# Optimization experiments

Hardware: AMD Instinct MI355X
Metric: run time of the kernel (lower is better)

Reference implementation:

```python
import jax, jax.numpy as jnp
import numpy as np

B, S, C = 16, 1024, 8
V, D, E, H, R = 50257, 512, 8, 512, 32
F, RT, CD, Q = 1024, 512, 64, 128
EPS = 1e-6


def _normalize(x):
    n = jnp.maximum(jnp.linalg.norm(x, axis=-1, keepdims=True), EPS)
    return x / n


def _fake_quantize(x):
    # F.normalize then straight-through int8 quant on the unit vector
    xn = _normalize(x)
    q = jnp.clip(jnp.round(xn * 127.0), -127.0, 127.0)
    return xn + jax.lax.stop_gradient(q / 127.0 - xn)


def setup_inputs() -> dict:
    key = jax.random.key(0)
    ks = iter(jax.random.split(key, 64))

    def w(shape, s=0.02):
        return (jax.random.normal(next(ks), shape, dtype=jnp.float32) * s)

    inp = {}
    inp['prefix_tokens'] = jax.random.randint(next(ks), (B, S), 0, V, dtype=jnp.int32)
    inp['chunk_inputs'] = jax.random.randint(next(ks), (B, C), 0, V, dtype=jnp.int32)
    inp['chunk_targets'] = jax.random.randint(next(ks), (B, C), 0, V, dtype=jnp.int32)
    inp['next_chunk_tokens'] = jax.random.randint(next(ks), (B, C), 0, V, dtype=jnp.int32)

    inp['emb'] = w((V, D))
    # stacked per-expert AffineExpert params
    inp['Wa'] = w((E, D, H)); inp['ba'] = jnp.zeros((E, H), jnp.float32)
    inp['Wg'] = w((E, D, R)); inp['bg'] = jnp.zeros((E, R), jnp.float32)
    inp['Wu'] = w((E, D, H)); inp['bu'] = jnp.zeros((E, H), jnp.float32)
    inp['u_mat'] = w((E, H, R)); inp['v_mat'] = w((E, H, R))
    inp['Wp'] = w((E, H, F)); inp['bp'] = jnp.zeros((E, F), jnp.float32)
    # gate MLP
    inp['Wg1'] = w((D, D)); inp['bg1'] = jnp.zeros((D,), jnp.float32)
    inp['Wg2'] = w((D, E)); inp['bg2'] = jnp.zeros((E,), jnp.float32)
    # query / target / key / code-expansion / write-code
    inp['Wq'] = w((F, Q)); inp['bq'] = jnp.zeros((Q,), jnp.float32)
    inp['Wt1'] = w((2 * D, RT)); inp['bt1'] = jnp.zeros((RT,), jnp.float32)
    inp['Wt2'] = w((RT, RT)); inp['bt2'] = jnp.zeros((RT,), jnp.float32)
    inp['Wk'] = w((RT, Q)); inp['bk'] = jnp.zeros((Q,), jnp.float32)
    inp['Web'] = w((CD, RT))  # expansion_basis (no bias)
    inp['Wwc'] = w((F, CD)); inp['bwc'] = jnp.zeros((CD,), jnp.float32)
    # ctx MLP
    inp['Wc1'] = w((2 * F, F)); inp['bc1'] = jnp.zeros((F,), jnp.float32)
    inp['Wc2'] = w((F, F)); inp['bc2'] = jnp.zeros((F,), jnp.float32)
    # chunk decoder
    inp['chunk_pos'] = w((C, F))
    inp['Wci'] = w((D + F, F)); inp['bci'] = jnp.zeros((F,), jnp.float32)
    inp['Wm1'] = w((F, F)); inp['bm1'] = jnp.zeros((F,), jnp.float32)
    inp['Wm2'] = w((F, F)); inp['bm2'] = jnp.zeros((F,), jnp.float32)
    inp['Wlm'] = w((F, V)); inp['blm'] = jnp.zeros((V,), jnp.float32)
    return inp


def _expert_scan(x, Wa, ba, Wg, bg, Wu, bu, u_mat, v_mat):
    # x: [B,S,D]; precompute all per-step projections as one big GEMM each,
    # leading axis = time for lax.scan. A,U: [S,E,B,H], G: [S,E,B,R]
    A = jax.nn.sigmoid(jnp.einsum('bsd,edh->sebh', x, Wa) + ba[None, :, None, :])
    G = jnp.einsum('bsd,edr->sebr', x, Wg) + bg[None, :, None, :]
    U = jnp.einsum('bsd,edh->sebh', x, Wu) + bu[None, :, None, :]

    def step(state, inp):  # state: [E,B,H]
        a, g, u = inp
        low = jnp.einsum('ebh,ehr->ebr', state, v_mat) * g
        state = a * state + u + jnp.einsum('ebr,ehr->ebh', low, u_mat)
        return state, None

    state0 = jnp.zeros((E, B, H), x.dtype)
    state, _ = jax.lax.scan(step, state0, (A, G, U))
    return state  # [E,B,H]


def reference(prefix_tokens, chunk_inputs, chunk_targets, next_chunk_tokens,
              emb, Wa, ba, Wg, bg, Wu, bu, u_mat, v_mat, Wp, bp,
              Wg1, bg1, Wg2, bg2, Wq, bq, Wt1, bt1, Wt2, bt2, Wk, bk,
              Web, Wwc, bwc, Wc1, bc1, Wc2, bc2,
              chunk_pos, Wci, bci, Wm1, bm1, Wm2, bm2, Wlm, blm):
    # ---- encode_prefix ----
    prefix_emb = emb[prefix_tokens]                       # [B,S,D]
    summary = prefix_emb.mean(axis=1)                     # [B,D]
    gate_probs = jax.nn.softmax(jax.nn.silu(summary @ Wg1 + bg1) @ Wg2 + bg2, axis=-1)  # [B,E]
    states = _expert_scan(prefix_emb, Wa, ba, Wg, bg, Wu, bu, u_mat, v_mat)             # [E,B,H]
    proj = jnp.einsum('ebh,ehf->ebf', states, Wp) + bp[:, None, :]                       # [E,B,F]
    fused = jnp.einsum('ebf,be->bf', proj, gate_probs)    # [B,F]

    # ---- query / target / key ----
    q_st = _fake_quantize(fused @ Wq + bq)                # [B,Q]
    chunk_emb = emb[chunk_targets].mean(axis=1)           # [B,D]
    next_emb = emb[next_chunk_tokens].mean(axis=1)        # [B,D]
    t_in = jnp.concatenate([chunk_emb, next_emb], axis=-1)
    target_state = _normalize(jax.nn.silu(t_in @ Wt1 + bt1) @ Wt2 + bt2)  # [B,RT]
    target_k_st = _fake_quantize(target_state @ Wk + bk)  # [B,Q]

    # ---- read_context (bank=None path -> zero read) ----
    zero_read = jnp.zeros_like(fused)
    c_in = jnp.concatenate([fused, zero_read], axis=-1)
    ctx = jax.nn.silu(c_in @ Wc1 + bc1) @ Wc2 + bc2       # [B,F]

    # ---- write_from_ctx ----
    write_codes = ctx @ Wwc + bwc                         # [B,CD]
    write_state = _normalize(write_codes @ Web)           # [B,RT]
    write_k_st = _fake_quantize(write_state @ Wk + bk)    # [B,Q]

    # ---- decode_chunk ----
    tok = emb[chunk_inputs]                               # [B,C,D]
    ctx_rep = jnp.broadcast_to(ctx[:, None, :], (B, C, F))
    hidden = jnp.concatenate([tok, ctx_rep], axis=-1) @ Wci + bci + chunk_pos[None]  # [B,C,F]
    hidden = jax.nn.silu(hidden @ Wm1 + bm1) @ Wm2 + bm2
    logits = hidden @ Wlm + blm                           # [B,C,V]

    # ---- losses ----
    logp = jax.nn.log_softmax(logits, axis=-1)
    token_loss = -jnp.take_along_axis(logp, chunk_targets[..., None], axis=-1)[..., 0]
    loss_nll = token_loss.mean()
    sim = (q_st @ target_k_st.T) / jnp.sqrt(jnp.float32(Q))  # [B,B]
    return logits, loss_nll, sim, write_k_st
```

## Files before the change

kernel.cpp:

```cpp
#include <hip/hip_runtime.h>
#include <math.h>

constexpr int BB = 16;
constexpr int SS = 1024;
constexpr int CC = 8;
constexpr int VV = 50257;
constexpr int DD = 512;
constexpr int EE = 8;
constexpr int HH = 512;
constexpr int RR = 32;
constexpr int FF = 1024;
constexpr int RTd = 512;
constexpr int CDd = 64;
constexpr int QQ = 128;
constexpr int SCH = 128;

typedef short bf16x8 __attribute__((ext_vector_type(8)));
typedef float f32x4 __attribute__((ext_vector_type(4)));

__device__ __forceinline__ float sigm(float x){ return 1.0f/(1.0f+expf(-x)); }

__device__ __forceinline__ unsigned short f2bf(float f){
  unsigned int u = __float_as_uint(f);
  u += 0x7fff + ((u>>16)&1);
  return (unsigned short)(u>>16);
}
__device__ __forceinline__ float bf2f(unsigned short h){
  return __uint_as_float(((unsigned int)h)<<16);
}

__device__ __forceinline__ void gload16(unsigned short* l, const unsigned short* g){
  __builtin_amdgcn_global_load_lds(
      (const __attribute__((address_space(1))) unsigned int*)(g),
      (__attribute__((address_space(3))) unsigned int*)(l), 16, 0, 0);
}

__global__ __launch_bounds__(256) void gather_pack(const int* __restrict__ toks,
    const float* __restrict__ emb, unsigned short* __restrict__ xp){
  int id = blockIdx.x*256 + threadIdx.x;
  int b = id >> 17;
  int rem = id & 131071;
  int c = rem >> 14;
  int rem2 = rem & 16383;
  int kc = rem2 >> 10;
  int pb = rem2 & 1023;
  int row = pb >> 3, q = pb & 7;
  int v = q ^ (row & 7);
  int kq = v >> 1, h = v & 1;
  int tok = toks[b*SS + c*128 + row];
  const float* src = emb + (size_t)tok*DD + kc*32 + kq*8;
  unsigned short o[8];
  #pragma unroll
  for (int j=0;j<8;j++){
    float f = src[j];
    unsigned short hi = f2bf(f);
    o[j] = h ? f2bf(f - bf2f(hi)) : hi;
  }
  ushort4* dst = (ushort4*)(xp + (size_t)id*8);
  dst[0] = make_ushort4(o[0],o[1],o[2],o[3]);
  dst[1] = make_ushort4(o[4],o[5],o[6],o[7]);
}

__global__ __launch_bounds__(512) void colsum_part(const int* __restrict__ toks,
    const float* __restrict__ emb, float* __restrict__ part){
  int b = blockIdx.y, j = blockIdx.x, d = threadIdx.x;
  float s = 0.f;
  for (int k=0;k<64;k++){
    int tok = toks[b*SS + j*64 + k];
    s += emb[(size_t)tok*DD + d];
  }
  part[(b*16 + j)*DD + d] = s;
}
__global__ __launch_bounds__(512) void colsum_final(const float* __restrict__ part,
                                                    float* __restrict__ summary){
  int b = blockIdx.x, d = threadIdx.x;
  float s = 0.f;
  for (int j=0;j<16;j++) s += part[(b*16 + j)*DD + d];
  summary[b*DD + d] = s * (1.0f/1024.0f);
}

__global__ __launch_bounds__(128) void gate_h1(const float* __restrict__ summary,
                                               const float* __restrict__ Wg1,
                                               const float* __restrict__ bg1,
                                               float* __restrict__ h1){
  int t = threadIdx.x; int j = blockIdx.x*128 + t;
  __shared__ float sm[16*512];
  for (int idx=t; idx<8192; idx+=128) sm[idx] = summary[idx];
  __syncthreads();
  float acc[16] = {0};
  for (int d=0; d<DD; d++){
    float w = Wg1[d*DD + j];
    #pragma unroll
    for (int b2=0;b2<16;b2++) acc[b2] += sm[b2*DD + d]*w;
  }
  #pragma unroll
  for (int b2=0;b2<16;b2++){ float v = acc[b2] + bg1[j]; h1[b2*DD + j] = v*sigm(v); }
}
__global__ __launch_bounds__(128) void gate_probs_k(const float* __restrict__ h1,
                                                    const float* __restrict__ Wg2,
                                                    const float* __restrict__ bg2,
                                                    float* __restrict__ gate){
  int t = threadIdx.x;
  int b = t>>3, e = t&7;
  float acc = bg2[e];
  for (int d=0; d<DD; d++) acc += h1[b*DD + d]*Wg2[d*EE + e];
  __shared__ float lg[16][8];
  lg[b][e] = acc;
  __syncthreads();
  if (e==0){
    float m = -3.4e38f;
    for (int i=0;i<8;i++) m = fmaxf(m, lg[b][i]);
    float s = 0.f; float ex[8];
    for (int i=0;i<8;i++){ ex[i] = expf(lg[b][i]-m); s += ex[i]; }
    for (int i=0;i<8;i++) gate[b*EE + i] = ex[i]/s;
  }
}

__global__ __launch_bounds__(256) void convT_pack_au(const float* __restrict__ Wa,
    const float* __restrict__ Wu, unsigned short* __restrict__ WPackAU){
  const int ec = blockIdx.x;
  const int kc = blockIdx.y;
  const int e = ec >> 3, ct = ec & 7;
  __shared__ float ta[32][64];
  __shared__ float tu[32][64];
  const int t = threadIdx.x;
  for (int i=0;i<8;i++){
    int id = t + i*256;
    int c = id & 63, kk = id >> 6;
    size_t src = ((size_t)e*DD + kc*32 + kk)*HH + ct*64 + c;
    ta[kk][c] = Wa[src];
    tu[kk][c] = Wu[src];
  }
  __syncthreads();
  unsigned short* o = WPackAU + ((size_t)ec*16 + kc)*8192;
  for (int i=0;i<8;i++){
    int idx4 = t + i*256;
    int blk = idx4 >> 1, half = idx4 & 1;
    int a = blk >> 8, kq = (blk >> 6) & 3, c = blk & 63;
    const float* src = (a >> 1) ? &tu[0][0] : &ta[0][0];
    unsigned short s4[4];
    #pragma unroll
    for (int j2=0;j2<4;j2++){
      int j = half*4 + j2;
      float f = src[(kq*8 + j)*64 + c];
      unsigned short hi = f2bf(f);
      s4[j2] = (a & 1) ? f2bf(f - bf2f(hi)) : hi;
    }
    *(ushort4*)&o[(size_t)idx4*4] = make_ushort4(s4[0],s4[1],s4[2],s4[3]);
  }
}
__global__ __launch_bounds__(256) void convT_pack_g(const float* __restrict__ Wge,
    unsigned short* __restrict__ WPackG){
  const int gt = blockIdx.x;
  const int kc = blockIdx.y;
  __shared__ float tg[32][64];
  const int t = threadIdx.x;
  for (int i=0;i<8;i++){
    int id = t + i*256;
    int c = id & 63, kk = id >> 6;
    int gcol = gt*64 + c;
    tg[kk][c] = Wge[((size_t)(gcol>>5)*DD + kc*32 + kk)*RR + (gcol & 31)];
  }
  __syncthreads();
  unsigned short* o = WPackG + ((size_t)gt*16 + kc)*4096;
  for (int i=0;i<4;i++){
    int idx4 = t + i*256;
    int blk = idx4 >> 1, half = idx4 & 1;
    int a = blk >> 8, kq = (blk >> 6) & 3, c = blk & 63;
    unsigned short s4[4];
    #pragma unroll
    for (int j2=0;j2<4;j2++){
      int j = half*4 + j2;
      float f = tg[kq*8 + j][c];
      unsigned short hi = f2bf(f);
      s4[j2] = a ? f2bf(f - bf2f(hi)) : hi;
    }
    *(ushort4*)&o[(size_t)idx4*4] = make_ushort4(s4[0],s4[1],s4[2],s4[3]);
  }
}

__global__ __launch_bounds__(512, 2) void aug_scan(
    const unsigned short* __restrict__ xp,
    const unsigned short* __restrict__ WPackAU, const unsigned short* __restrict__ WPackG,
    const float* __restrict__ ba, const float* __restrict__ bu, const float* __restrict__ bge,
    float* __restrict__ Aw, float* __restrict__ Uw, float* __restrict__ Gw,
    const float* __restrict__ Ar, const float* __restrict__ Ur, const float* __restrict__ Gr,
    const float* __restrict__ v_mat, const float* __restrict__ u_mat,
    float* __restrict__ states,
    int s0, int do_aug, int do_scan)
{
  __shared__ __align__(16) unsigned short lds[32768];
  const int t = threadIdx.x;
  const int xcd  = blockIdx.x & 7;
  const int slot = blockIdx.x >> 3;

  if (slot < 16){
    if (!do_scan) return;
    const int e = xcd;
    const int b = slot;
    const int r = t & 31, grp = t >> 5;
    float* stf   = (float*)lds;
    float* partf = (float*)lds + 1024;
    float* lowf  = (float*)lds + 1312;
    float vreg[32];
    #pragma unroll
    for (int i=0;i<32;i++) vreg[i] = v_mat[((size_t)e*HH + grp*32 + i)*RR + r];
    float ureg[32];
    {
      const float4* up = (const float4*)(u_mat + ((size_t)e*HH + t)*RR);
      #pragma unroll
      for (int j=0;j<8;j++){
        float4 v4 = up[j];
        ureg[j*4+0]=v4.x; ureg[j*4+1]=v4.y; ureg[j*4+2]=v4.z; ureg[j*4+3]=v4.w;
      }
    }
    const size_t sbase = ((size_t)e*BB + b)*HH + t;
    const size_t abase = ((size_t)e*BB + b)*SCH*HH + t;
    const size_t gbase = ((size_t)e*BB + b)*SCH*RR + r;
    float streg = states[sbase];
    stf[t] = streg;
    float a0 = Ar[abase], u0 = Ur[abase];
    float g0 = (t < 32) ? Gr[gbase] : 0.f;
    float a1 = Ar[abase + HH], u1 = Ur[abase + HH];
    float g1 = (t < 32) ? Gr[gbase + RR] : 0.f;
    __syncthreads();
    int cur = 0;
    for (int s=0; s<SCH; s++){
      float a2 = 0.f, u2 = 0.f, g2 = 0.f;
      if (s+2 < SCH){
        a2 = Ar[abase + (size_t)(s+2)*HH];
        u2 = Ur[abase + (size_t)(s+2)*HH];
        if (t < 32) g2 = Gr[gbase + (size_t)(s+2)*RR];
      }
      {
        const float* sp = &stf[cur*512 + grp*32];
        float p0=0.f,p1=0.f,p2=0.f,p3=0.f;
        #pragma unroll
        for (int i=0;i<8;i++){
          p0 += sp[i]     *vreg[i];
          p1 += sp[8+i]   *vreg[8+i];
          p2 += sp[16+i]  *vreg[16+i];
          p3 += sp[24+i]  *vreg[24+i];
        }
        float p = (p0+p1)+(p2+p3);
        p += __shfl_xor(p, 32, 64);
        if ((t & 32) == 0) partf[r*9 + (grp>>1)] = p;
      }
      __syncthreads();
      if (t < 32){
        float ss2 = 0.f;
        #pragma unroll
        for (int j=0;j<8;j++) ss2 += partf[t*9 + j];
        lowf[t] = ss2 * g0;
      }
      __syncthreads();
      {
        float q0=0.f,q1=0.f,q2=0.f,q3=0.f;
        #pragma unroll
        for (int i=0;i<8;i++){
          q0 += lowf[i]   *ureg[i];
          q1 += lowf[8+i] *ureg[8+i];
          q2 += lowf[16+i]*ureg[16+i];
          q3 += lowf[24+i]*ureg[24+i];
        }
        streg = a0*streg + u0 + ((q0+q1)+(q2+q3));
      }
      stf[(cur^1)*512 + t] = streg;
      cur ^= 1;
      a0=a1; u0=u1; g0=g1; a1=a2; u1=u2; g1=g2;
      __syncthreads();
    }
    states[sbase] = streg;
    return;
  }

  if (!do_aug) return;
  const int s2 = slot - 16;
  int b, ct;
  if (s2 < 128){ ct = xcd*8 + (s2 & 7); b = s2 >> 3; }
  else         { ct = 64 + (xcd >> 1);  b = ((xcd & 1) << 3) + (s2 - 128); }
  const int lane = t & 63, wv = t >> 6;
  const int cix = s0 >> 7;
  const unsigned short* xpc = xp + (((size_t)(b*8 + cix)) << 17);
  const int wo = wv*64;

  f32x4 acc[2][4] = {};
  const int cl15 = lane & 15;

  if (ct < 64){
    const int e = ct >> 3;
    const int c0 = (ct & 7)*64;
    const unsigned short* wpc = WPackAU + (((size_t)ct) << 17);
    const int strip = wv & 3;
    const int mode  = wv >> 2;
    const int kq4 = lane >> 4;
    const int rr0 = strip*32 + cl15, rr1 = rr0 + 16;
    const int qh = (kq4*2) ^ (rr0 & 7);
    const int ql = (kq4*2+1) ^ (rr0 & 7);
    const int ab = mode*512;

#define STAGE_AU(BUF, KC) { \
    unsigned short* XB_ = lds + (BUF)*16384; \
    unsigned short* WB_ = XB_ + 8192; \
    const unsigned short* gx = xpc + (KC)*8192; \
    const unsigned short* gw = wpc + (KC)*8192; \
    gload16(XB_ + wo*8,        gx + (size_t)(wo + lane)*8); \
    gload16(XB_ + (512+wo)*8,  gx + (size_t)(512 + wo + lane)*8); \
    gload16(WB_ + wo*8,        gw + (size_t)(wo + lane)*8); \
    gload16(WB_ + (512+wo)*8,  gw + (size_t)(512 + wo + lane)*8); }

    STAGE_AU(0, 0)
    asm volatile("s_waitcnt vmcnt(0)" ::: "memory");
    __builtin_amdgcn_s_barrier();
    __builtin_amdgcn_sched_barrier(0);
    int cur = 0;
    for (int kc=0; kc<16; kc++){
      if (kc < 15) STAGE_AU(cur^1, kc+1)
      const unsigned short* XB = lds + cur*16384;
      const unsigned short* WB = XB + 8192;
      bf16x8 ah0 = *(const bf16x8*)&XB[(rr0*8 + qh)*8];
      bf16x8 al0 = *(const bf16x8*)&XB[(rr0*8 + ql)*8];
      bf16x8 ah1 = *(const bf16x8*)&XB[(rr1*8 + qh)*8];
      bf16x8 al1 = *(const bf16x8*)&XB[(rr1*8 + ql)*8];
      #pragma unroll
      for (int cf=0; cf<4; cf++){
        const int cc = cf*16 + cl15;
        bf16x8 bh = *(const bf16x8*)&WB[(ab + kq4*64 + cc)*8];
        bf16x8 bl = *(const bf16x8*)&WB[(ab + 256 + kq4*64 + cc)*8];
        acc[0][cf] = __builtin_amdgcn_mfma_f32_16x16x32_bf16(ah0, bh, acc[0][cf], 0,0,0);
        acc[0][cf] = __builtin_amdgcn_mfma_f32_16x16x32_bf16(ah0, bl, acc[0][cf], 0,0,0);
        acc[0][cf] = __builtin_amdgcn_mfma_f32_16x16x32_bf16(al0, bh, acc[0][cf], 0,0,0);
        acc[1][cf] = __builtin_amdgcn_mfma_f32_16x16x32_bf16(ah1, bh, acc[1][cf], 0,0,0);
        acc[1][cf] = __builtin_amdgcn_mfma_f32_16x16x32_bf16(ah1, bl, acc[1][cf], 0,0,0);
        acc[1][cf] = __builtin_amdgcn_mfma_f32_16x16x32_bf16(al1, bh, acc[1][cf], 0,0,0);
      }
      __builtin_amdgcn_sched_barrier(0);
      asm volatile("s_waitcnt vmcnt(0)" ::: "memory");
      __builtin_amdgcn_s_barrier();
      __builtin_amdgcn_sched_barrier(0);
      cur ^= 1;
    }
#undef STAGE_AU
    const int r4 = (lane >> 4) * 4;
    const size_t obase = ((size_t)e*BB + b)*SCH*HH;
    #pragma unroll
    for (int rf=0; rf<2; rf++){
      #pragma unroll
      for (int cf=0; cf<4; cf++){
        #pragma unroll
        for (int i=0;i<4;i++){
          int sl = strip*32 + rf*16 + r4 + i;
          int ce = c0 + cf*16 + cl15;
          float v = acc[rf][cf][i];
          if (mode == 0){
            v += ba[e*HH + ce];
            v = sigm(v);
            Aw[obase + (size_t)sl*HH + ce] = v;
          } else {
            v += bu[e*HH + ce];
            Uw[obase + (size_t)sl*HH + ce] = v;
          }
        }
      }
    }
  } else {
    const int gt = ct - 64;
    const int c0 = gt*64;
    const unsigned short* wpc = WPackG + (((size_t)gt) << 16);
    const int kq4 = lane >> 4;
    const int rr0 = wv*16 + cl15;
    const int qh = (kq4*2) ^ (rr0 & 7);
    const int ql = (kq4*2+1) ^ (rr0 & 7);

#define STAGE_G(BUF, KC) { \
    unsigned short* XB_ = lds + (BUF)*16384; \
    unsigned short* WB_ = XB_ + 8192; \
    const unsigned short* gx = xpc + (KC)*8192; \
    const unsigned short* gw = wpc + (KC)*4096; \
    gload16(XB_ + wo*8,        gx + (size_t)(wo + lane)*8); \
    gload16(XB_ + (512+wo)*8,  gx + (size_t)(512 + wo + lane)*8); \
    gload16(WB_ + wo*8,        gw + (size_t)(wo + lane)*8); }

    STAGE_G(0, 0)
    asm volatile("s_waitcnt vmcnt(0)" ::: "memory");
    __builtin_amdgcn_s_barrier();
    __builtin_amdgcn_sched_barrier(0);
    int cur = 0;
    for (int kc=0; kc<16; kc++){
      if (kc < 15) STAGE_G(cur^1, kc+1)
      const unsigned short* XB = lds + cur*16384;
      const unsigned short* WB = XB + 8192;
      bf16x8 ah0 = *(const bf16x8*)&XB[(rr0*8 + qh)*8];
      bf16x8 al0 = *(const bf16x8*)&XB[(rr0*8 + ql)*8];
      #pragma unroll
      for (int cf=0; cf<4; cf++){
        const int cc = cf*16 + cl15;
        bf16x8 bh = *(const bf16x8*)&WB[(kq4*64 + cc)*8];
        bf16x8 bl = *(const bf16x8*)&WB[(256 + kq4*64 + cc)*8];
        acc[0][cf] = __builtin_amdgcn_mfma_f32_16x16x32_bf16(ah0, bh, acc[0][cf], 0,0,0);
        acc[0][cf] = __builtin_amdgcn_mfma_f32_16x16x32_bf16(ah0, bl, acc[0][cf], 0,0,0);
        acc[0][cf] = __builtin_amdgcn_mfma_f32_16x16x32_bf16(al0, bh, acc[0][cf], 0,0,0);
      }
      __builtin_amdgcn_sched_barrier(0);
      asm volatile("s_waitcnt vmcnt(0)" ::: "memory");
      __builtin_amdgcn_s_barrier();
      __builtin_amdgcn_sched_barrier(0);
      cur ^= 1;
    }
#undef STAGE_G
    const int r4 = (lane >> 4) * 4;
    #pragma unroll
    for (int cf=0; cf<4; cf++){
      #pragma unroll
      for (int i=0;i<4;i++){
        int sl = wv*16 + r4 + i;
        int g = c0 + cf*16 + cl15;
        int ee = g >> 5, r2 = g & 31;
        float v = acc[0][cf][i] + bge[ee*RR + r2];
        Gw[((size_t)ee*BB + b)*SCH*RR + (size_t)sl*RR + r2] = v;
      }
    }
  }
}

__global__ __launch_bounds__(128) void proj_partial(const float* __restrict__ states,
    const float* __restrict__ Wp, const float* __restrict__ gate, float* __restrict__ pf){
  int fc = blockIdx.x, e = blockIdx.y, t = threadIdx.x;
  __shared__ float stl[16*512];
  for (int idx=t; idx<8192; idx+=128) stl[idx] = states[(size_t)e*8192 + idx];
  __syncthreads();
  int f = fc*128 + t;
  float acc[16] = {0};
  for (int h=0; h<HH; h++){
    float w = Wp[((size_t)e*HH + h)*FF + f];
    #pragma unroll
    for (int b2=0;b2<16;b2++) acc[b2] += stl[b2*HH + h]*w;
  }
  #pragma unroll
  for (int b2=0;b2<16;b2++) pf[((size_t)(e*16 + b2))*FF + f] = gate[b2*EE + e]*acc[b2];
}
__global__ __launch_bounds__(256) void fuse_reduce(const float* __restrict__ pf,
    const float* __restrict__ gate, const float* __restrict__ bp, float* __restrict__ fused){
  int idx = blockIdx.x*256 + threadIdx.x;
  int b = idx >> 10, f = idx & 1023;
  float s = 0.f;
  #pragma unroll
  for (int e=0;e<8;e++) s += pf[((size_t)(e*16 + b))*FF + f] + gate[b*EE + e]*bp[e*FF + f];
  fused[idx] = s;
}

__global__ __launch_bounds__(128) void fq_linear(const float* __restrict__ in, int Kin,
    const float* __restrict__ W, const float* __restrict__ bias, float* __restrict__ out){
  int b = blockIdx.x, t = threadIdx.x;
  __shared__ float xin[1024];
  __shared__ float red[2];
  for (int k=t;k<Kin;k+=128) xin[k] = in[(size_t)b*Kin + k];
  __syncthreads();
  float acc = bias[t];
  for (int k=0;k<Kin;k++) acc += xin[k]*W[k*QQ + t];
  float ss = acc*acc;
  #pragma unroll
  for (int off=32; off; off>>=1) ss += __shfl_xor(ss, off, 64);
  if ((t&63)==0) red[t>>6] = ss;
  __syncthreads();
  float n = fmaxf(sqrtf(red[0]+red[1]), 1e-6f);
  float xn = acc / n;
  float q = fminf(fmaxf(rintf(xn*127.0f), -127.0f), 127.0f) * (1.0f/127.0f);
  out[b*QQ + t] = q;
}

__global__ __launch_bounds__(512) void chunk_means(const int* __restrict__ ct,
    const int* __restrict__ nct, const float* __restrict__ emb, float* __restrict__ tin){
  int b = blockIdx.x, d = threadIdx.x;
  float ce=0.f, ne=0.f;
  for (int c=0;c<CC;c++){
    ce += emb[(size_t)ct[b*CC+c]*DD + d];
    ne += emb[(size_t)nct[b*CC+c]*DD + d];
  }
  tin[b*1024 + d] = ce*0.125f;
  tin[b*1024 + 512 + d] = ne*0.125f;
}

__global__ __launch_bounds__(512) void target_state_kernel(const float* __restrict__ tin,
    const float* __restrict__ Wt1, const float* __restrict__ bt1,
    const float* __restrict__ Wt2, const float* __restrict__ bt2, float* __restrict__ outts){
  int b = blockIdx.x, t = threadIdx.x;
  __shared__ float xin[1024];
  __shared__ float h1[512];
  __shared__ float red[8];
  for (int k=t;k<1024;k+=512) xin[k] = tin[b*1024 + k];
  __syncthreads();
  float acc = bt1[t];
  for (int k=0;k<1024;k++) acc += xin[k]*Wt1[k*RTd + t];
  acc = acc*sigm(acc);
  h1[t] = acc;
  __syncthreads();
  float y = bt2[t];
  for (int k=0;k<512;k++) y += h1[k]*Wt2[k*RTd + t];
  float ss = y*y;
  #pragma unroll
  for (int off=32; off; off>>=1) ss += __shfl_xor(ss, off, 64);
  if ((t&63)==0) red[t>>6] = ss;
  __syncthreads();
  float tot = 0.f;
  #pragma unroll
  for (int i=0;i<8;i++) tot += red[i];
  float n = fmaxf(sqrtf(tot), 1e-6f);
  outts[b*RTd + t] = y/n;
}

__global__ __launch_bounds__(512) void write_state_kernel(const float* __restrict__ ctx,
    const float* __restrict__ Wwc, const float* __restrict__ bwc,
    const float* __restrict__ Web, float* __restrict__ wsn){
  int b = blockIdx.x, t = threadIdx.x;
  __shared__ float cx[1024];
  __shared__ float wc[64];
  __shared__ float red[8];
  for (int k=t;k<1024;k+=512) cx[k] = ctx[b*FF + k];
  __syncthreads();
  if (t < 64){
    float a = bwc[t];
    for (int k=0;k<1024;k++) a += cx[k]*Wwc[k*CDd + t];
    wc[t] = a;
  }
  __syncthreads();
  float y = 0.f;
  for (int k=0;k<64;k++) y += wc[k]*Web[k*RTd + t];
  float ss = y*y;
  #pragma unroll
  for (int off=32; off; off>>=1) ss += __shfl_xor(ss, off, 64);
  if ((t&63)==0) red[t>>6] = ss;
  __syncthreads();
  float tot = 0.f;
  #pragma unroll
  for (int i=0;i<8;i++) tot += red[i];
  float n = fmaxf(sqrtf(tot), 1e-6f);
  wsn[b*RTd + t] = y/n;
}

__global__ __launch_bounds__(256) void sim_kernel(const float* __restrict__ q,
    const float* __restrict__ k, float* __restrict__ out){
  int t = threadIdx.x;
  int i = t>>4, j = t&15;
  float s = 0.f;
  for (int c=0;c<QQ;c++) s += q[i*QQ + c]*k[j*QQ + c];
  out[t] = s / sqrtf(128.0f);
}

__global__ __launch_bounds__(256) void build_xcat(const int* __restrict__ ci,
    const float* __restrict__ emb, const float* __restrict__ ctx, float* __restrict__ xcat){
  int idx = blockIdx.x*256 + threadIdx.x;
  int row = idx / 1536, k = idx % 1536;
  float v = (k < DD) ? emb[(size_t)ci[row]*DD + k] : ctx[(row>>3)*FF + (k - DD)];
  xcat[idx] = v;
}

__global__ __launch_bounds__(256) void gemm_part(const float* __restrict__ X,
    const float* __restrict__ W, float* __restrict__ part,
    int K, int KS, int M){
  const int t = threadIdx.x;
  const int col = blockIdx.x*64 + (t & 63);
  const int r0 = blockIdx.y*16;
  const int ks = blockIdx.z;
  const int rg = t >> 6;
  const int kslice = K / KS;
  const int kbeg = ks*kslice;
  __shared__ float xs[16][65];
  float acc[4] = {};
  for (int k0=kbeg; k0<kbeg+kslice; k0+=64){
    #pragma unroll
    for (int i=0;i<4;i++){
      int id = t + i*256;
// ... 87 lines not shown
      bf16x8 al1 = *(const bf16x8*)&xsl[(rr1*8 + (kq4^(rr1&7)))*8];
      #pragma unroll
      for (int cf=0; cf<4; cf++){
        const int cc = cf*16 + (lane&15);
        bf16x8 bh = *(const bf16x8*)&wsh[(kq4*64 + cc)*8];
        bf16x8 bl = *(const bf16x8*)&wsl[(kq4*64 + cc)*8];
        acc[0][cf] = __builtin_amdgcn_mfma_f32_16x16x32_bf16(ah0, bh, acc[0][cf], 0,0,0);
        acc[0][cf] = __builtin_amdgcn_mfma_f32_16x16x32_bf16(ah0, bl, acc[0][cf], 0,0,0);
        acc[0][cf] = __builtin_amdgcn_mfma_f32_16x16x32_bf16(al0, bh, acc[0][cf], 0,0,0);
        acc[1][cf] = __builtin_amdgcn_mfma_f32_16x16x32_bf16(ah1, bh, acc[1][cf], 0,0,0);
        acc[1][cf] = __builtin_amdgcn_mfma_f32_16x16x32_bf16(ah1, bl, acc[1][cf], 0,0,0);
        acc[1][cf] = __builtin_amdgcn_mfma_f32_16x16x32_bf16(al1, bh, acc[1][cf], 0,0,0);
      }
    }
    __syncthreads();
  }
  const int cl = lane & 15;
  const int r4 = (lane >> 4) * 4;
  #pragma unroll
  for (int rf=0; rf<2; rf++){
    #pragma unroll
    for (int cf=0; cf<4; cf++){
      int c = cb + cf*16 + cl;
      if (c >= VV) continue;
      float bb = blm[c];
      #pragma unroll
      for (int i=0;i<4;i++){
        int row = w*32 + rf*16 + r4 + i;
        out[(size_t)row*VV + c] = acc[rf][cf][i] + bb;
      }
    }
  }
}

__global__ __launch_bounds__(512) void softmax_nll(const float* __restrict__ logits,
    const int* __restrict__ tgt, float* __restrict__ tl){
  const int row = blockIdx.x;
  const float* p = logits + (size_t)row*VV;
  const int t = threadIdx.x;
  float m = -3.4e38f, s = 0.f;
  for (int c=t; c<VV; c+=512){
    float v = p[c];
    if (v > m){ s = s*expf(m - v) + 1.0f; m = v; }
    else s += expf(v - m);
  }
  #pragma unroll
  for (int off=32; off; off>>=1){
    float m2 = __shfl_xor(m, off, 64);
    float s2 = __shfl_xor(s, off, 64);
    float mn = fmaxf(m, m2);
    s = s*expf(m - mn) + s2*expf(m2 - mn);
    m = mn;
  }
  __shared__ float ms[8], ssh[8];
  if ((t&63)==0){ ms[t>>6] = m; ssh[t>>6] = s; }
  __syncthreads();
  if (t==0){
    float M = ms[0], S = ssh[0];
    for (int i=1;i<8;i++){
      float mn = fmaxf(M, ms[i]);
      S = S*expf(M-mn) + ssh[i]*expf(ms[i]-mn);
      M = mn;
    }
    tl[row] = M + logf(S) - p[tgt[row]];
  }
}
__global__ __launch_bounds__(128) void loss_reduce(const float* __restrict__ tl,
                                                   float* __restrict__ out){
  int t = threadIdx.x;
  float v = tl[t];
  #pragma unroll
  for (int off=32; off; off>>=1) v += __shfl_xor(v, off, 64);
  __shared__ float r2[2];
  if ((t&63)==0) r2[t>>6] = v;
  __syncthreads();
  if (t==0) out[0] = (r2[0]+r2[1]) * (1.0f/128.0f);
}

extern "C" void kernel_launch(void* const* d_in, const int* in_sizes, int n_in,
                              void* d_out, int out_size, void* d_ws, size_t ws_size,
                              hipStream_t stream){
  (void)in_sizes; (void)n_in; (void)out_size;
  const int*  prefix = (const int*)d_in[0];
  const int*  cinp   = (const int*)d_in[1];
  const int*  ctgt   = (const int*)d_in[2];
  const int*  nctk   = (const int*)d_in[3];
  const float* emb  = (const float*)d_in[4];
  const float* Wa   = (const float*)d_in[5];
  const float* ba   = (const float*)d_in[6];
  const float* Wge  = (const float*)d_in[7];
  const float* bge  = (const float*)d_in[8];
  const float* Wu   = (const float*)d_in[9];
  const float* bu   = (const float*)d_in[10];
  const float* u_mat= (const float*)d_in[11];
  const float* v_mat= (const float*)d_in[12];
  const float* Wp   = (const float*)d_in[13];
  const float* bp   = (const float*)d_in[14];
  const float* Wg1  = (const float*)d_in[15];
  const float* bg1  = (const float*)d_in[16];
  const float* Wg2  = (const float*)d_in[17];
  const float* bg2  = (const float*)d_in[18];
  const float* Wq   = (const float*)d_in[19];
  const float* bq   = (const float*)d_in[20];
  const float* Wt1  = (const float*)d_in[21];
  const float* bt1  = (const float*)d_in[22];
  const float* Wt2  = (const float*)d_in[23];
  const float* bt2  = (const float*)d_in[24];
  const float* Wk   = (const float*)d_in[25];
  const float* bk   = (const float*)d_in[26];
  const float* Web  = (const float*)d_in[27];
  const float* Wwc  = (const float*)d_in[28];
  const float* bwc  = (const float*)d_in[29];
  const float* Wc1  = (const float*)d_in[30];
  const float* bc1  = (const float*)d_in[31];
  const float* Wc2  = (const float*)d_in[32];
  const float* bc2  = (const float*)d_in[33];
  const float* cpos = (const float*)d_in[34];
  const float* Wci  = (const float*)d_in[35];
  const float* bci  = (const float*)d_in[36];
  const float* Wm1  = (const float*)d_in[37];
  const float* bm1  = (const float*)d_in[38];
  const float* Wm2  = (const float*)d_in[39];
  const float* bm2  = (const float*)d_in[40];
  const float* Wlm  = (const float*)d_in[41];
  const float* blm  = (const float*)d_in[42];

  float* ws = (float*)d_ws;
  size_t off = 0;
  unsigned short* xp = (unsigned short*)(ws + off); off += (size_t)BB*SS*DD;
  float* Abuf0  = ws + off; off += (size_t)SCH*EE*BB*HH;
  float* Ubuf0  = ws + off; off += (size_t)SCH*EE*BB*HH;
  float* Gbuf0  = ws + off; off += (size_t)SCH*EE*BB*RR;
  float* statesb= ws + off; off += (size_t)EE*BB*HH;
  float* partb  = ws + off; off += (size_t)BB*16*DD;
  float* summb  = ws + off; off += (size_t)BB*DD;
  float* h1b    = ws + off; off += (size_t)BB*DD;
  float* gateb  = ws + off; off += (size_t)BB*EE;
  float* pfb    = ws + off; off += (size_t)EE*BB*FF;
  float* fusedb = ws + off; off += (size_t)BB*FF;
  float* qstb   = ws + off; off += (size_t)BB*QQ;
  float* tinb   = ws + off; off += (size_t)BB*2*DD;
  float* tstb   = ws + off; off += (size_t)BB*RTd;
  float* tkb    = ws + off; off += (size_t)BB*QQ;
  float* ctxb   = ws + off; off += (size_t)BB*FF;
  float* hctxb  = ws + off; off += (size_t)BB*FF;
  float* wsnb   = ws + off; off += (size_t)BB*RTd;
  float* xcatb  = ws + off; off += (size_t)BB*CC*(DD+FF);
  float* hid1b  = ws + off; off += (size_t)BB*CC*FF;
  float* h2b    = ws + off; off += (size_t)BB*CC*FF;
  float* hidb   = ws + off; off += (size_t)BB*CC*FF;
  float* tlb    = ws + off; off += (size_t)BB*CC;
  float* ppart  = ws + off; off += (size_t)4*BB*CC*FF;
  unsigned short* WPackAU = (unsigned short*)(ws + off); off += (size_t)EE*DD*HH*2;
  unsigned short* WPackG  = (unsigned short*)(ws + off); off += (size_t)EE*DD*RR;
  unsigned short* hhb  = (unsigned short*)(ws + off); off += (size_t)BB*CC*FF/2;
  unsigned short* hlb  = (unsigned short*)(ws + off); off += (size_t)BB*CC*FF/2;
  float* Abuf1  = ws + off; off += (size_t)SCH*EE*BB*HH;
  float* Ubuf1  = ws + off; off += (size_t)SCH*EE*BB*HH;
  float* Gbuf1  = ws + off; off += (size_t)SCH*EE*BB*RR;
  const bool fused = ws_size >= off * sizeof(float);

  float* out = (float*)d_out;
  const size_t LOGITS_OFF = 0;
  const size_t LOSS_OFF = (size_t)BB*CC*VV;
  const size_t SIM_OFF  = LOSS_OFF + 1;
  const size_t WK_OFF   = SIM_OFF + (size_t)BB*BB;

  convT_pack_au<<<dim3(64,16), 256, 0, stream>>>(Wa, Wu, WPackAU);
  convT_pack_g<<<dim3(4,16), 256, 0, stream>>>(Wge, WPackG);

  gather_pack<<<8192, 256, 0, stream>>>(prefix, emb, xp);
  colsum_part<<<dim3(16,16), 512, 0, stream>>>(prefix, emb, partb);
  colsum_final<<<16, 512, 0, stream>>>(partb, summb);
  gate_h1<<<4, 128, 0, stream>>>(summb, Wg1, bg1, h1b);
  gate_probs_k<<<1, 128, 0, stream>>>(h1b, Wg2, bg2, gateb);

  hipMemsetAsync(statesb, 0, (size_t)EE*BB*HH*sizeof(float), stream);

  if (fused){
    for (int c=0; c<=8; c++){
      int da = (c<8) ? 1 : 0;
      int dscn = (c>=1) ? 1 : 0;
      float* Aw = (c&1) ? Abuf1 : Abuf0;
      float* Uw = (c&1) ? Ubuf1 : Ubuf0;
      float* Gw = (c&1) ? Gbuf1 : Gbuf0;
      const float* Ar = ((c-1)&1) ? Abuf1 : Abuf0;
      const float* Ur = ((c-1)&1) ? Ubuf1 : Ubuf0;
      const float* Gr = ((c-1)&1) ? Gbuf1 : Gbuf0;
      int grid = da ? 1216 : 128;
      aug_scan<<<grid, 512, 0, stream>>>(xp, WPackAU, WPackG, ba, bu, bge,
          Aw, Uw, Gw, Ar, Ur, Gr, v_mat, u_mat, statesb,
          c*SCH, da, dscn);
    }
  } else {
    for (int c=0; c<8; c++){
      aug_scan<<<1216, 512, 0, stream>>>(xp, WPackAU, WPackG, ba, bu, bge,
          Abuf0, Ubuf0, Gbuf0, Abuf0, Ubuf0, Gbuf0, v_mat, u_mat, statesb,
          c*SCH, 1, 0);
      aug_scan<<<128, 512, 0, stream>>>(xp, WPackAU, WPackG, ba, bu, bge,
          Abuf0, Ubuf0, Gbuf0, Abuf0, Ubuf0, Gbuf0, v_mat, u_mat, statesb,
          c*SCH, 0, 1);
    }
  }

  proj_partial<<<dim3(8,8), 128, 0, stream>>>(statesb, Wp, gateb, pfb);
  fuse_reduce<<<64, 256, 0, stream>>>(pfb, gateb, bp, fusedb);

  fq_linear<<<16, 128, 0, stream>>>(fusedb, FF, Wq, bq, qstb);
  chunk_means<<<16, 512, 0, stream>>>(ctgt, nctk, emb, tinb);
  target_state_kernel<<<16, 512, 0, stream>>>(tinb, Wt1, bt1, Wt2, bt2, tstb);
  fq_linear<<<16, 128, 0, stream>>>(tstb, RTd, Wk, bk, tkb);

  gemm_part<<<dim3(16,1,4), 256, 0, stream>>>(fusedb, Wc1, ppart, FF, 4, 16);
  gemm_combine<<<64, 256, 0, stream>>>(ppart, bc1, nullptr, hctxb, 4, 16, 1);
  gemm_part<<<dim3(16,1,4), 256, 0, stream>>>(hctxb, Wc2, ppart, FF, 4, 16);
  gemm_combine<<<64, 256, 0, stream>>>(ppart, bc2, nullptr, ctxb, 4, 16, 0);

  write_state_kernel<<<16, 512, 0, stream>>>(ctxb, Wwc, bwc, Web, wsnb);
  fq_linear<<<16, 128, 0, stream>>>(wsnb, RTd, Wk, bk, out + WK_OFF);
  sim_kernel<<<1, 256, 0, stream>>>(qstb, tkb, out + SIM_OFF);

  build_xcat<<<768, 256, 0, stream>>>(cinp, emb, ctxb, xcatb);
  gemm_part<<<dim3(16,8,4), 256, 0, stream>>>(xcatb, Wci, ppart, DD+FF, 4, 128);
  gemm_combine<<<512, 256, 0, stream>>>(ppart, bci, cpos, hid1b, 4, 128, 0);
  gemm_part<<<dim3(16,8,4), 256, 0, stream>>>(hid1b, Wm1, ppart, FF, 4, 128);
  gemm_combine<<<512, 256, 0, stream>>>(ppart, bm1, nullptr, h2b, 4, 128, 1);
  gemm_part<<<dim3(16,8,4), 256, 0, stream>>>(h2b, Wm2, ppart, FF, 4, 128);
  gemm_combine<<<512, 256, 0, stream>>>(ppart, bm2, nullptr, hidb, 4, 128, 0);

  split_h<<<512, 256, 0, stream>>>(hidb, hhb, hlb);
  logits_mfma<<<(VV+63)/64, 256, 0, stream>>>(hhb, hlb, Wlm, blm, out + LOGITS_OFF);

  softmax_nll<<<BB*CC, 512, 0, stream>>>(out + LOGITS_OFF, ctgt, tlb);
  loss_reduce<<<1, 128, 0, stream>>>(tlb, out + LOSS_OFF);
}
```

Measured before the change: 1.700 ms.

## Retile expert affine GEMM: keep activation chunk in LDS, stream weights directly

Restructures the per-chunk A/U/G projection inside aug_scan. Each block now loads a 64-row (or 32-row for G) slab of the packed activations for all 16 K-chunks into a doubled 128KB LDS buffer. Each wave then reads pre-packed bf16 hi/lo weight fragments straight from global memory into registers, replacing the double-buffered LDS staging of both operands. The weight packing kernels are rewritten to emit the new per-wave fragment layout, and the aug grid shrinks from 1216 to 448 blocks with larger per-block tiles. The goal is fewer barriers and less redundant activation traffic. The costs are more accumulator registers, LDS usage that limits occupancy, and weight loads that now go through global/L2 without LDS staging.

```diff
diff --git a/kernel.cpp b/kernel.cpp
--- a/kernel.cpp
+++ b/kernel.cpp
@@ -118,70 +118,71 @@
 
 __global__ __launch_bounds__(256) void convT_pack_au(const float* __restrict__ Wa,
     const float* __restrict__ Wu, unsigned short* __restrict__ WPackAU){
-  const int ec = blockIdx.x;
-  const int kc = blockIdx.y;
-  const int e = ec >> 3, ct = ec & 7;
-  __shared__ float ta[32][64];
-  __shared__ float tu[32][64];
+  const int bid = blockIdx.x;
+  const int e = bid >> 5;
+  const int au = (bid >> 4) & 1;
+  const int kc = bid & 15;
+  const float* W = (au ? Wu : Wa) + (size_t)e*DD*HH + (size_t)kc*32*HH;
+  __shared__ float tw[32][513];
   const int t = threadIdx.x;
+  for (int i=0;i<64;i++){
+    int id = t + i*256;
+    int c = id & 511, k = id >> 9;
+    tw[k][c] = W[(size_t)k*HH + c];
+  }
+  __syncthreads();
+  for (int i=0;i<16;i++){
+    int slot = t + i*256;
+    int wq = slot >> 10, rem = slot & 1023;
+    int cf = rem >> 7, hl = (rem >> 6) & 1, lane = rem & 63;
+    int col = wq*128 + cf*16 + (lane & 15);
+    int kb = lane >> 4;
+    unsigned short o[8];
+    #pragma unroll
+    for (int j=0;j<8;j++){
+      float f = tw[kb*8 + j][col];
+      unsigned short hi = f2bf(f);
+      o[j] = hl ? f2bf(f - bf2f(hi)) : hi;
+    }
+    size_t dst = (size_t)(e*2+au)*524288 + (size_t)(wq*16 + kc)*8192
+               + (size_t)(cf*2 + hl)*512 + lane*8;
+    *(ushort4*)&WPackAU[dst]   = make_ushort4(o[0],o[1],o[2],o[3]);
+    *(ushort4*)&WPackAU[dst+4] = make_ushort4(o[4],o[5],o[6],o[7]);
+  }
+}
+__global__ __launch_bounds__(256) void convT_pack_g(const float* __restrict__ Wge,
+    unsigned short* __restrict__ WPG){
+  const int kc = blockIdx.x;
+  __shared__ float tg[32][257];
+  const int t = threadIdx.x;
+  for (int i=0;i<32;i++){
+    int id = t + i*256;
+    int r = id & 31, k = (id >> 5) & 31, e = id >> 10;
+    tg[k][e*32 + r] = Wge[((size_t)e*DD + kc*32 + k)*RR + r];
+  }
+  __syncthreads();
   for (int i=0;i<8;i++){
-    int id = t + i*256;
-    int c = id & 63, kk = id >> 6;
-    size_t src = ((size_t)e*DD + kc*32 + kk)*HH + ct*64 + c;
-    ta[kk][c] = Wa[src];
-    tu[kk][c] = Wu[src];
-  }
-  __syncthreads();
-  unsigned short* o = WPackAU + ((size_t)ec*16 + kc)*8192;
-  for (int i=0;i<8;i++){
-    int idx4 = t + i*256;
-    int blk = idx4 >> 1, half = idx4 & 1;
-    int a = blk >> 8, kq = (blk >> 6) & 3, c = blk & 63;
-    const float* src = (a >> 1) ? &tu[0][0] : &ta[0][0];
-    unsigned short s4[4];
-    #pragma unroll
-    for (int j2=0;j2<4;j2++){
-      int j = half*4 + j2;
-      float f = src[(kq*8 + j)*64 + c];
+    int slot = t + i*256;
+    int w = slot >> 8, rem = slot & 255;
+    int cf = rem >> 7, hl = (rem >> 6) & 1, lane = rem & 63;
+    int gcol = w*32 + cf*16 + (lane & 15);
+    int kb = lane >> 4;
+    unsigned short o[8];
+    #pragma unroll
+    for (int j=0;j<8;j++){
+      float f = tg[kb*8 + j][gcol];
       unsigned short hi = f2bf(f);
-      s4[j2] = (a & 1) ? f2bf(f - bf2f(hi)) : hi;
-    }
-    *(ushort4*)&o[(size_t)idx4*4] = make_ushort4(s4[0],s4[1],s4[2],s4[3]);
-  }
-}
-__global__ __launch_bounds__(256) void convT_pack_g(const float* __restrict__ Wge,
-    unsigned short* __restrict__ WPackG){
-  const int gt = blockIdx.x;
-  const int kc = blockIdx.y;
-  __shared__ float tg[32][64];
-  const int t = threadIdx.x;
-  for (int i=0;i<8;i++){
-    int id = t + i*256;
-    int c = id & 63, kk = id >> 6;
-    int gcol = gt*64 + c;
-    tg[kk][c] = Wge[((size_t)(gcol>>5)*DD + kc*32 + kk)*RR + (gcol & 31)];
-  }
-  __syncthreads();
-  unsigned short* o = WPackG + ((size_t)gt*16 + kc)*4096;
-  for (int i=0;i<4;i++){
-    int idx4 = t + i*256;
-    int blk = idx4 >> 1, half = idx4 & 1;
-    int a = blk >> 8, kq = (blk >> 6) & 3, c = blk & 63;
-    unsigned short s4[4];
-    #pragma unroll
-    for (int j2=0;j2<4;j2++){
-      int j = half*4 + j2;
-      float f = tg[kq*8 + j][c];
-      unsigned short hi = f2bf(f);
-      s4[j2] = a ? f2bf(f - bf2f(hi)) : hi;
-    }
-    *(ushort4*)&o[(size_t)idx4*4] = make_ushort4(s4[0],s4[1],s4[2],s4[3]);
+      o[j] = hl ? f2bf(f - bf2f(hi)) : hi;
+    }
+    size_t dst = (((size_t)(w*16 + kc)*2 + cf)*2 + hl)*512 + lane*8;
+    *(ushort4*)&WPG[dst]   = make_ushort4(o[0],o[1],o[2],o[3]);
+    *(ushort4*)&WPG[dst+4] = make_ushort4(o[4],o[5],o[6],o[7]);
   }
 }
 
 __global__ __launch_bounds__(512, 2) void aug_scan(
     const unsigned short* __restrict__ xp,
-    const unsigned short* __restrict__ WPackAU, const unsigned short* __restrict__ WPackG,
+    const unsigned short* __restrict__ WPackAU, const unsigned short* __restrict__ WPG,
     const float* __restrict__ ba, const float* __restrict__ bu, const float* __restrict__ bge,
     float* __restrict__ Aw, float* __restrict__ Uw, float* __restrict__ Gw,
     const float* __restrict__ Ar, const float* __restrict__ Ur, const float* __restrict__ Gr,
@@ -189,7 +190,7 @@
     float* __restrict__ states,
     int s0, int do_aug, int do_scan)
 {
-  __shared__ __align__(16) unsigned short lds[32768];
+  __shared__ __align__(16) unsigned short lds[65536];
   const int t = threadIdx.x;
   const int xcd  = blockIdx.x & 7;
   const int slot = blockIdx.x >> 3;
@@ -237,10 +238,10 @@
         float p0=0.f,p1=0.f,p2=0.f,p3=0.f;
         #pragma unroll
         for (int i=0;i<8;i++){
-          p0 += sp[i]     *vreg[i];
-          p1 += sp[8+i]   *vreg[8+i];
-          p2 += sp[16+i]  *vreg[16+i];
-          p3 += sp[24+i]  *vreg[24+i];
+          p0 += sp[i]    *vreg[i];
+          p1 += sp[8+i]  *vreg[8+i];
+          p2 += sp[16+i] *vreg[16+i];
+          p3 += sp[24+i] *vreg[24+i];
         }
         float p = (p0+p1)+(p2+p3);
         p += __shfl_xor(p, 32, 64);
@@ -275,149 +276,142 @@
   }
 
   if (!do_aug) return;
-  const int s2 = slot - 16;
-  int b, ct;
-  if (s2 < 128){ ct = xcd*8 + (s2 & 7); b = s2 >> 3; }
-  else         { ct = 64 + (xcd >> 1);  b = ((xcd & 1) << 3) + (s2 - 128); }
   const int lane = t & 63, wv = t >> 6;
+  const int cl15 = lane & 15;
+  const int kb = lane >> 4;
   const int cix = s0 >> 7;
-  const unsigned short* xpc = xp + (((size_t)(b*8 + cix)) << 17);
-  const int wo = wv*64;
-
-  f32x4 acc[2][4] = {};
-  const int cl15 = lane & 15;
-
-  if (ct < 64){
-    const int e = ct >> 3;
-    const int c0 = (ct & 7)*64;
-    const unsigned short* wpc = WPackAU + (((size_t)ct) << 17);
-    const int strip = wv & 3;
-    const int mode  = wv >> 2;
-    const int kq4 = lane >> 4;
-    const int rr0 = strip*32 + cl15, rr1 = rr0 + 16;
-    const int qh = (kq4*2) ^ (rr0 & 7);
-    const int ql = (kq4*2+1) ^ (rr0 & 7);
-    const int ab = mode*512;
-
-#define STAGE_AU(BUF, KC) { \
-    unsigned short* XB_ = lds + (BUF)*16384; \
-    unsigned short* WB_ = XB_ + 8192; \
-    const unsigned short* gx = xpc + (KC)*8192; \
-    const unsigned short* gw = wpc + (KC)*8192; \
-    gload16(XB_ + wo*8,        gx + (size_t)(wo + lane)*8); \
-    gload16(XB_ + (512+wo)*8,  gx + (size_t)(512 + wo + lane)*8); \
-    gload16(WB_ + wo*8,        gw + (size_t)(wo + lane)*8); \
-    gload16(WB_ + (512+wo)*8,  gw + (size_t)(512 + wo + lane)*8); }
-
-    STAGE_AU(0, 0)
-    asm volatile("s_waitcnt vmcnt(0)" ::: "memory");
-    __builtin_amdgcn_s_barrier();
-    __builtin_amdgcn_sched_barrier(0);
-    int cur = 0;
-    for (int kc=0; kc<16; kc++){
-      if (kc < 15) STAGE_AU(cur^1, kc+1)
-      const unsigned short* XB = lds + cur*16384;
-      const unsigned short* WB = XB + 8192;
-      bf16x8 ah0 = *(const bf16x8*)&XB[(rr0*8 + qh)*8];
-      bf16x8 al0 = *(const bf16x8*)&XB[(rr0*8 + ql)*8];
-      bf16x8 ah1 = *(const bf16x8*)&XB[(rr1*8 + qh)*8];
-      bf16x8 al1 = *(const bf16x8*)&XB[(rr1*8 + ql)*8];
-      #pragma unroll
-      for (int cf=0; cf<4; cf++){
-        const int cc = cf*16 + cl15;
-        bf16x8 bh = *(const bf16x8*)&WB[(ab + kq4*64 + cc)*8];
-        bf16x8 bl = *(const bf16x8*)&WB[(ab + 256 + kq4*64 + cc)*8];
-        acc[0][cf] = __builtin_amdgcn_mfma_f32_16x16x32_bf16(ah0, bh, acc[0][cf], 0,0,0);
-        acc[0][cf] = __builtin_amdgcn_mfma_f32_16x16x32_bf16(ah0, bl, acc[0][cf], 0,0,0);
-        acc[0][cf] = __builtin_amdgcn_mfma_f32_16x16x32_bf16(al0, bh, acc[0][cf], 0,0,0);
-        acc[1][cf] = __builtin_amdgcn_mfma_f32_16x16x32_bf16(ah1, bh, acc[1][cf], 0,0,0);
-        acc[1][cf] = __builtin_amdgcn_mfma_f32_16x16x32_bf16(ah1, bl, acc[1][cf], 0,0,0);
-        acc[1][cf] = __builtin_amdgcn_mfma_f32_16x16x32_bf16(al1, bh, acc[1][cf], 0,0,0);
-      }
-      __builtin_amdgcn_sched_barrier(0);
-      asm volatile("s_waitcnt vmcnt(0)" ::: "memory");
-      __builtin_amdgcn_s_barrier();
-      __builtin_amdgcn_sched_barrier(0);
-      cur ^= 1;
-    }
-#undef STAGE_AU
-    const int r4 = (lane >> 4) * 4;
-    const size_t obase = ((size_t)e*BB + b)*SCH*HH;
-    #pragma unroll
-    for (int rf=0; rf<2; rf++){
-      #pragma unroll
-      for (int cf=0; cf<4; cf++){
+
+  if (slot < 48){
+    const int e = xcd;
+    const int idx = slot - 16;
+    const int b = idx & 15;
+    const int r0 = (idx >> 4) * 64;
+    const unsigned short* xpc = xp + (((size_t)(b*8 + cix)) << 17);
+    const int au = wv >> 2, wq = wv & 3;
+    const unsigned short* wb = WPackAU + (size_t)(e*2+au)*524288 + (size_t)wq*16*8192;
+
+    {
+      const int kc = wv;
+      const unsigned short* src = xpc + kc*8192 + r0*64;
+      unsigned short* dst = lds + kc*4096;
+      #pragma unroll
+      for (int i=0;i<8;i++)
+        gload16(dst + i*512, src + (size_t)(i*64 + lane)*8);
+    }
+    __syncthreads();
+    {
+      const int kc = 8 + wv;
+      const unsigned short* src = xpc + kc*8192 + r0*64;
+      unsigned short* dst = lds + kc*4096;
+      #pragma unroll
+      for (int i=0;i<8;i++)
+        gload16(dst + i*512, src + (size_t)(i*64 + lane)*8);
+    }
+
+    f32x4 acc[4][8] = {};
+    for (int half=0; half<2; half++){
+      if (half) __syncthreads();
+      for (int kc = half*8; kc < half*8 + 8; kc++){
+        bf16x8 ah[4], al[4];
+        #pragma unroll
+        for (int rf=0; rf<4; rf++){
+          const int rloc = rf*16 + cl15;
+          const int qh = (kb*2) ^ (rloc & 7);
+          ah[rf] = *(const bf16x8*)&lds[kc*4096 + rloc*64 + qh*8];
+          al[rf] = *(const bf16x8*)&lds[kc*4096 + rloc*64 + (qh^1)*8];
+        }
+        #pragma unroll
+        for (int cf=0; cf<8; cf++){
+          const unsigned short* fp = wb + ((size_t)kc*8 + cf)*1024 + lane*8;
+          bf16x8 bh = *(const bf16x8*)fp;
+          bf16x8 bl = *(const bf16x8*)(fp + 512);
+          #pragma unroll
+          for (int rf=0; rf<4; rf++){
+            acc[rf][cf] = __builtin_amdgcn_mfma_f32_16x16x32_bf16(ah[rf], bh, acc[rf][cf], 0,0,0);
+            acc[rf][cf] = __builtin_amdgcn_mfma_f32_16x16x32_bf16(ah[rf], bl, acc[rf][cf], 0,0,0);
+            acc[rf][cf] = __builtin_amdgcn_mfma_f32_16x16x32_bf16(al[rf], bh, acc[rf][cf], 0,0,0);
+          }
+        }
+      }
+    }
+    const float* bias = au ? bu : ba;
+    float* dst = (au ? Uw : Aw) + ((size_t)(e*BB + b)*SCH + r0)*HH;
+    #pragma unroll
+    for (int rf=0; rf<4; rf++){
+      #pragma unroll
+      for (int cf=0; cf<8; cf++){
+        const int col = wq*128 + cf*16 + cl15;
+        const float bv = bias[e*HH + col];
         #pragma unroll
         for (int i=0;i<4;i++){
-          int sl = strip*32 + rf*16 + r4 + i;
-          int ce = c0 + cf*16 + cl15;
-          float v = acc[rf][cf][i];
-          if (mode == 0){
-            v += ba[e*HH + ce];
-            v = sigm(v);
-            Aw[obase + (size_t)sl*HH + ce] = v;
-          } else {
-            v += bu[e*HH + ce];
-            Uw[obase + (size_t)sl*HH + ce] = v;
+          const int rloc = rf*16 + (lane>>4)*4 + i;
+          float v = acc[rf][cf][i] + bv;
+          if (!au) v = sigm(v);
+          dst[(size_t)rloc*HH + col] = v;
+        }
+      }
+    }
+  } else {
+    const int idx2 = slot - 48;
+    const int b = (xcd << 1) | (idx2 & 1);
+    const int r0 = (idx2 >> 1) * 32;
+    const unsigned short* xpc = xp + (((size_t)(b*8 + cix)) << 17);
+    {
+      const int kc = wv;
+      const unsigned short* src = xpc + kc*8192 + r0*64;
+      unsigned short* dst = lds + kc*2048;
+      #pragma unroll
+      for (int i=0;i<4;i++)
+        gload16(dst + i*512, src + (size_t)(i*64 + lane)*8);
+    }
+    __syncthreads();
+    {
+      const int kc = 8 + wv;
+      const unsigned short* src = xpc + kc*8192 + r0*64;
+      unsigned short* dst = lds + kc*2048;
+      #pragma unroll
+      for (int i=0;i<4;i++)
+        gload16(dst + i*512, src + (size_t)(i*64 + lane)*8);
+    }
+    f32x4 acc[2][2] = {};
+    const unsigned short* wb = WPG + (size_t)wv*32768;
+    for (int half=0; half<2; half++){
+      if (half) __syncthreads();
+      for (int kc = half*8; kc < half*8 + 8; kc++){
+        bf16x8 ah[2], al[2];
+        #pragma unroll
+        for (int rf=0; rf<2; rf++){
+          const int rloc = rf*16 + cl15;
+          const int qh = (kb*2) ^ (rloc & 7);
+          ah[rf] = *(const bf16x8*)&lds[kc*2048 + rloc*64 + qh*8];
+          al[rf] = *(const bf16x8*)&lds[kc*2048 + rloc*64 + (qh^1)*8];
+        }
+        #pragma unroll
+        for (int cf=0; cf<2; cf++){
+          const unsigned short* fp = wb + ((size_t)kc*2 + cf)*1024 + lane*8;
+          bf16x8 bh = *(const bf16x8*)fp;
+          bf16x8 bl = *(const bf16x8*)(fp + 512);
+          #pragma unroll
+          for (int rf=0; rf<2; rf++){
+            acc[rf][cf] = __builtin_amdgcn_mfma_f32_16x16x32_bf16(ah[rf], bh, acc[rf][cf], 0,0,0);
+            acc[rf][cf] = __builtin_amdgcn_mfma_f32_16x16x32_bf16(ah[rf], bl, acc[rf][cf], 0,0,0);
+            acc[rf][cf] = __builtin_amdgcn_mfma_f32_16x16x32_bf16(al[rf], bh, acc[rf][cf], 0,0,0);
           }
         }
       }
     }
-  } else {
-    const int gt = ct - 64;
-    const int c0 = gt*64;
-    const unsigned short* wpc = WPackG + (((size_t)gt) << 16);
-    const int kq4 = lane >> 4;
-    const int rr0 = wv*16 + cl15;
-    const int qh = (kq4*2) ^ (rr0 & 7);
-    const int ql = (kq4*2+1) ^ (rr0 & 7);
-
-#define STAGE_G(BUF, KC) { \
-    unsigned short* XB_ = lds + (BUF)*16384; \
-    unsigned short* WB_ = XB_ + 8192; \
-    const unsigned short* gx = xpc + (KC)*8192; \
-    const unsigned short* gw = wpc + (KC)*4096; \
-    gload16(XB_ + wo*8,        gx + (size_t)(wo + lane)*8); \
-    gload16(XB_ + (512+wo)*8,  gx + (size_t)(512 + wo + lane)*8); \
-    gload16(WB_ + wo*8,        gw + (size_t)(wo + lane)*8); }
-
-    STAGE_G(0, 0)
-    asm volatile("s_waitcnt vmcnt(0)" ::: "memory");
-    __builtin_amdgcn_s_barrier();
-    __builtin_amdgcn_sched_barrier(0);
-    int cur = 0;
-    for (int kc=0; kc<16; kc++){
-      if (kc < 15) STAGE_G(cur^1, kc+1)
-      const unsigned short* XB = lds + cur*16384;
-      const unsigned short* WB = XB + 8192;
-      bf16x8 ah0 = *(const bf16x8*)&XB[(rr0*8 + qh)*8];
-      bf16x8 al0 = *(const bf16x8*)&XB[(rr0*8 + ql)*8];
-      #pragma unroll
-      for (int cf=0; cf<4; cf++){
-        const int cc = cf*16 + cl15;
-        bf16x8 bh = *(const bf16x8*)&WB[(kq4*64 + cc)*8];
-        bf16x8 bl = *(const bf16x8*)&WB[(256 + kq4*64 + cc)*8];
-        acc[0][cf] = __builtin_amdgcn_mfma_f32_16x16x32_bf16(ah0, bh, acc[0][cf], 0,0,0);
-        acc[0][cf] = __builtin_amdgcn_mfma_f32_16x16x32_bf16(ah0, bl, acc[0][cf], 0,0,0);
-        acc[0][cf] = __builtin_amdgcn_mfma_f32_16x16x32_bf16(al0, bh, acc[0][cf], 0,0,0);
-      }
-      __builtin_amdgcn_sched_barrier(0);
-      asm volatile("s_waitcnt vmcnt(0)" ::: "memory");
-      __builtin_amdgcn_s_barrier();
-      __builtin_amdgcn_sched_barrier(0);
-      cur ^= 1;
-    }
-#undef STAGE_G
-    const int r4 = (lane >> 4) * 4;
-    #pragma unroll
-    for (int cf=0; cf<4; cf++){
-      #pragma unroll
-      for (int i=0;i<4;i++){
-        int sl = wv*16 + r4 + i;
-        int g = c0 + cf*16 + cl15;
-        int ee = g >> 5, r2 = g & 31;
-        float v = acc[0][cf][i] + bge[ee*RR + r2];
-        Gw[((size_t)ee*BB + b)*SCH*RR + (size_t)sl*RR + r2] = v;
+    #pragma unroll
+    for (int rf=0; rf<2; rf++){
+      #pragma unroll
+      for (int cf=0; cf<2; cf++){
+        const int gcol = wv*32 + cf*16 + cl15;
+        const int ee = gcol >> 5, r = gcol & 31;
+        const float bv = bge[ee*RR + r];
+        #pragma unroll
+        for (int i=0;i<4;i++){
+          const int rloc = rf*16 + (lane>>4)*4 + i;
+          Gw[((size_t)(ee*BB + b)*SCH + r0 + rloc)*RR + r] = acc[rf][cf][i] + bv;
+        }
       }
     }
   }
@@ -811,7 +805,7 @@
   float* tlb    = ws + off; off += (size_t)BB*CC;
   float* ppart  = ws + off; off += (size_t)4*BB*CC*FF;
   unsigned short* WPackAU = (unsigned short*)(ws + off); off += (size_t)EE*DD*HH*2;
-  unsigned short* WPackG  = (unsigned short*)(ws + off); off += (size_t)EE*DD*RR;
+  unsigned short* WPG     = (unsigned short*)(ws + off); off += (size_t)EE*DD*RR;
   unsigned short* hhb  = (unsigned short*)(ws + off); off += (size_t)BB*CC*FF/2;
   unsigned short* hlb  = (unsigned short*)(ws + off); off += (size_t)BB*CC*FF/2;
   float* Abuf1  = ws + off; off += (size_t)SCH*EE*BB*HH;
@@ -825,8 +819,8 @@
   const size_t SIM_OFF  = LOSS_OFF + 1;
   const size_t WK_OFF   = SIM_OFF + (size_t)BB*BB;
 
-  convT_pack_au<<<dim3(64,16), 256, 0, stream>>>(Wa, Wu, WPackAU);
-  convT_pack_g<<<dim3(4,16), 256, 0, stream>>>(Wge, WPackG);
+  convT_pack_au<<<256, 256, 0, stream>>>(Wa, Wu, WPackAU);
+  convT_pack_g<<<16, 256, 0, stream>>>(Wge, WPG);
 
   gather_pack<<<8192, 256, 0, stream>>>(prefix, emb, xp);
   colsum_part<<<dim3(16,16), 512, 0, stream>>>(prefix, emb, partb);
@@ -846,17 +840,17 @@
       const float* Ar = ((c-1)&1) ? Abuf1 : Abuf0;
       const float* Ur = ((c-1)&1) ? Ubuf1 : Ubuf0;
       const float* Gr = ((c-1)&1) ? Gbuf1 : Gbuf0;
-      int grid = da ? 1216 : 128;
-      aug_scan<<<grid, 512, 0, stream>>>(xp, WPackAU, WPackG, ba, bu, bge,
+      int grid = da ? 448 : 128;
+      aug_scan<<<grid, 512, 0, stream>>>(xp, WPackAU, WPG, ba, bu, bge,
           Aw, Uw, Gw, Ar, Ur, Gr, v_mat, u_mat, statesb,
           c*SCH, da, dscn);
     }
   } else {
     for (int c=0; c<8; c++){
-      aug_scan<<<1216, 512, 0, stream>>>(xp, WPackAU, WPackG, ba, bu, bge,
+      aug_scan<<<448, 512, 0, stream>>>(xp, WPackAU, WPG, ba, bu, bge,
           Abuf0, Ubuf0, Gbuf0, Abuf0, Ubuf0, Gbuf0, v_mat, u_mat, statesb,
           c*SCH, 1, 0);
-      aug_scan<<<128, 512, 0, stream>>>(xp, WPackAU, WPackG, ba, bu, bge,
+      aug_scan<<<128, 512, 0, stream>>>(xp, WPackAU, WPG, ba, bu, bge,
           Abuf0, Ubuf0, Gbuf0, Abuf0, Ubuf0, Gbuf0, v_mat, u_mat, statesb,
           c*SCH, 0, 1);
     }
```

Result: no change. 1.699 ms (-0.1%).
